# Performance work log

Hardware: AMD Instinct MI355X
Metric: run time of the kernel (lower is better)

The kernel has to match this reference:

```python
import jax, jax.numpy as jnp
import numpy as np
import math

S, B, D = 2048, 2, 1024
H = 16
DH = D // H
WIN = 256
DIL = 1


def setup_inputs() -> dict:
    key = jax.random.key(0)
    ks = jax.random.split(key, 10)
    std = 1.0 / math.sqrt(D)
    return {
        "x": jax.random.normal(ks[0], (S, B, D), jnp.float32),
        "beta": jax.random.normal(ks[1], (H,), jnp.float32) * 0.02,
        "Wq": jax.random.normal(ks[2], (D, D), jnp.float32) * std,
        "bq": jnp.zeros((D,), jnp.float32),
        "Wk": jax.random.normal(ks[3], (D, D), jnp.float32) * std,
        "bk": jnp.zeros((D,), jnp.float32),
        "Wv": jax.random.normal(ks[4], (D, D), jnp.float32) * std,
        "bv": jnp.zeros((D,), jnp.float32),
        "Wo": jax.random.normal(ks[5], (D, D), jnp.float32) * std,
        "bo": jnp.zeros((D,), jnp.float32),
    }


def _split_heads(t):
    # (S, B, D) -> (B*H, S, DH), matching rearrange 's b (h d) -> (b h) s d'
    return t.reshape(S, B, H, DH).transpose(1, 2, 0, 3).reshape(B * H, S, DH)


def reference(x, beta, Wq, bq, Wk, bk, Wv, bv, Wo, bo):
    q = _split_heads(x @ Wq + bq)
    k = _split_heads(x @ Wk + bk)
    v = _split_heads(x @ Wv + bv)

    # per-head learnable temperature: q / (sqrt(d_head) * exp(beta))
    beta_exp = jnp.tile(jnp.exp(beta), B)  # (B*H,), head index = z % H
    q = q / (jnp.sqrt(jnp.asarray(DH, x.dtype)) * beta_exp)[:, None, None]

    # causal dilated windowed mask
    idx = jnp.arange(S)
    diff = idx[:, None] - idx[None, :]
    allowed = (diff >= 0) & (diff <= DIL * (WIN - 1)) & (diff % DIL == 0)
    mask = jnp.where(allowed, jnp.asarray(0.0, x.dtype), jnp.asarray(-jnp.inf, x.dtype))

    scores = jnp.einsum('zqd,zkd->zqk', q, k) + mask[None]
    # attention sink: extra zero-logit column absorbing probability mass
    scores = jnp.concatenate([scores, jnp.zeros((B * H, S, 1), scores.dtype)], axis=-1)
    attn = jax.nn.softmax(scores, axis=-1)[..., :-1]

    out = jnp.einsum('zqk,zkd->zqd', attn, v)
    # (B*H, S, DH) -> (S, B, D)
    out = out.reshape(B, H, S, DH).transpose(2, 0, 1, 3).reshape(S, B, D)
    return out @ Wo + bo
```

## Files before the change

### kernel.cpp

```cpp
#include <hip/hip_runtime.h>
#include <math.h>

#define S_LEN  2048
#define BATCH  2
#define DM     1024
#define NHEAD  16
#define DHEAD  64
#define WIN    256
#define MROWS  4096

#define PPAD 68

#define BM 128
#define BN 96
#define BK 32
#define NKT (DM / BK)

#define OM 128
#define ON 64

typedef __attribute__((ext_vector_type(8))) short bf16x8;
typedef __attribute__((ext_vector_type(4))) float f32x4;

__device__ __forceinline__ unsigned short f2b(float f) {
    unsigned int u = __float_as_uint(f);
    return (unsigned short)((u + 0x7fffu + ((u >> 16) & 1u)) >> 16);
}
__device__ __forceinline__ void gld16(const void* g, void* l) {
    __builtin_amdgcn_global_load_lds(
        (const __attribute__((address_space(1))) void*)g,
        (__attribute__((address_space(3))) void*)l, 16, 0, 0);
}
__device__ __forceinline__ bf16x8 pack8(float4 a, float4 b) {
    bf16x8 r;
    r[0] = (short)f2b(a.x); r[1] = (short)f2b(a.y);
    r[2] = (short)f2b(a.z); r[3] = (short)f2b(a.w);
    r[4] = (short)f2b(b.x); r[5] = (short)f2b(b.y);
    r[6] = (short)f2b(b.z); r[7] = (short)f2b(b.w);
    return r;
}

__global__ __launch_bounds__(256)
void twcvt4(const float* __restrict__ W0, const float* __restrict__ W1,
            const float* __restrict__ W2, const float* __restrict__ W3,
            const float* __restrict__ x,
            unsigned short* __restrict__ T0, unsigned short* __restrict__ T1,
            unsigned short* __restrict__ T2, unsigned short* __restrict__ T3,
            unsigned short* __restrict__ xb)
{
    const int zz = blockIdx.z;
    if (zz == 4) {
        const int flat = blockIdx.y * 32 + blockIdx.x;
        const int base = flat * 4096 + threadIdx.x * 4;
#pragma unroll
        for (int p = 0; p < 4; ++p) {
            const int i = base + p * 1024;
            float4 f = *(const float4*)(x + i);
            ushort4 o;
            o.x = f2b(f.x); o.y = f2b(f.y); o.z = f2b(f.z); o.w = f2b(f.w);
            *(ushort4*)(xb + i) = o;
        }
        return;
    }
    const float* W = (zz == 0) ? W0 : (zz == 1) ? W1 : (zz == 2) ? W2 : W3;
    unsigned short* WT = (zz == 0) ? T0 : (zz == 1) ? T1 : (zz == 2) ? T2 : T3;

    __shared__ float t32[32][33];
    const int bx = blockIdx.x * 32;
    const int by = blockIdx.y * 32;
    const int c  = threadIdx.x & 31;
    const int r0 = threadIdx.x >> 5;
#pragma unroll
    for (int p = 0; p < 4; ++p)
        t32[r0 + 8 * p][c] = W[(size_t)(by + r0 + 8 * p) * DM + bx + c];
    __syncthreads();
#pragma unroll
    for (int p = 0; p < 4; ++p)
        WT[(size_t)(bx + r0 + 8 * p) * DM + by + c] = f2b(t32[c][r0 + 8 * p]);
}

__global__ __launch_bounds__(256, 4)
void gemm_qkv(const unsigned short* __restrict__ A,
              const unsigned short* __restrict__ BT,
              const float* __restrict__ b0,
              const float* __restrict__ b1,
              const float* __restrict__ b2,
              const float* __restrict__ beta,
              unsigned short* __restrict__ Cb)
{
    __shared__ unsigned short Ab[2][BM * BK];
    __shared__ unsigned short Bb[2][BN * BK];

    const int t   = threadIdx.x;
    const int ln  = t & 63;
    const int wv  = t >> 6;
    const int wr  = wv >> 1;
    const int wc  = wv & 1;
    const int m16 = ln & 15;
    const int g   = ln >> 4;
    const int swz = (m16 >> 1) & 3;

    const int rowBase = blockIdx.y * BM;
    const int colBase = blockIdx.x * BN;

    const int sr  = t >> 2;
    const int scx = (t & 3) ^ ((sr >> 1) & 3);
    const size_t gOff = (size_t)sr * DM + scx * 8;
    const int    ldOff = t * 8;

    f32x4 acc[4][3];
#pragma unroll
    for (int u = 0; u < 4; ++u)
#pragma unroll
        for (int v = 0; v < 3; ++v)
            acc[u][v] = (f32x4){0.f, 0.f, 0.f, 0.f};

    const unsigned short* aBase = A  + (size_t)rowBase * DM + gOff;
    const unsigned short* bBase = BT + (size_t)colBase * DM + gOff;

    {
        gld16(aBase,                    &Ab[0][ldOff]);
        gld16(aBase + (size_t)64 * DM,  &Ab[0][2048 + ldOff]);
        gld16(bBase,                    &Bb[0][ldOff]);
        if (t < 128)
            gld16(bBase + (size_t)64 * DM, &Bb[0][2048 + ldOff]);
        asm volatile("s_waitcnt vmcnt(0)" ::: "memory");
        __builtin_amdgcn_s_barrier();
        __builtin_amdgcn_sched_barrier(0);
    }

    for (int kt = 0; kt < NKT; ++kt) {
        const int cur = kt & 1;
        const unsigned short* Ac = Ab[cur];
        const unsigned short* Bc = Bb[cur];
        unsigned short* An = Ab[cur ^ 1];
        unsigned short* Bn = Bb[cur ^ 1];
        const bool hn = (kt < NKT - 1);
        const unsigned short* aS = aBase + (size_t)(kt + 1) * BK;
        const unsigned short* bS = bBase + (size_t)(kt + 1) * BK;

        if (hn) {
            gld16(aS,                   &An[ldOff]);
            gld16(aS + (size_t)64 * DM, &An[2048 + ldOff]);
            gld16(bS,                   &Bn[ldOff]);
            if (t < 128)
                gld16(bS + (size_t)64 * DM, &Bn[2048 + ldOff]);
        }

        bf16x8 af[4], bf[3];
#pragma unroll
        for (int u = 0; u < 4; ++u)
            af[u] = *(const bf16x8*)&Ac[(wr * 64 + u * 16 + m16) * BK + ((g ^ swz) * 8)];
#pragma unroll
        for (int v = 0; v < 3; ++v)
            bf[v] = *(const bf16x8*)&Bc[(wc * 48 + v * 16 + m16) * BK + ((g ^ swz) * 8)];

        __builtin_amdgcn_s_setprio(1);
#pragma unroll
        for (int u = 0; u < 4; ++u)
#pragma unroll
            for (int v = 0; v < 3; ++v)
                acc[u][v] = __builtin_amdgcn_mfma_f32_16x16x32_bf16(
                    af[u], bf[v], acc[u][v], 0, 0, 0);
        __builtin_amdgcn_s_setprio(0);

        if (hn)
            asm volatile("s_waitcnt vmcnt(0)" ::: "memory");
        __builtin_amdgcn_s_barrier();
        __builtin_amdgcn_sched_barrier(0);
    }

    const int q4 = g * 4;
#pragma unroll
    for (int v = 0; v < 3; ++v) {
        const int col = colBase + wc * 48 + v * 16 + m16;
        const int sec = col >> 10;
        const int h   = (col >> 6) & (NHEAD - 1);
        const int dh  = col & 63;
        if (sec < 2) {
            const float bi = (sec == 0 ? b0 : b1)[col & (DM - 1)];
            const float sc = (sec == 0) ? 0.125f * __expf(-beta[h]) : 1.0f;
            unsigned short* base = Cb + (size_t)sec * MROWS * DM;
#pragma unroll
            for (int u = 0; u < 4; ++u)
#pragma unroll
                for (int r = 0; r < 4; ++r) {
                    const int row = rowBase + wr * 64 + u * 16 + q4 + r;
                    const int s = row >> 1, bb = row & 1;
                    const int z = bb * NHEAD + h;
                    base[((size_t)z * S_LEN + s) * DHEAD + dh] =
                        f2b((acc[u][v][r] + bi) * sc);
                }
        } else {
            unsigned short* vtb = Cb + (size_t)2 * MROWS * DM;
            const float bi = b2[col & (DM - 1)];
#pragma unroll
            for (int u = 0; u < 4; ++u) {
                const int row0 = rowBase + wr * 64 + u * 16 + q4;
                const int s0   = row0 >> 1;
                ushort2 p0, p1;
                p0.x = f2b(acc[u][v][0] + bi);
                p0.y = f2b(acc[u][v][2] + bi);
                p1.x = f2b(acc[u][v][1] + bi);
                p1.y = f2b(acc[u][v][3] + bi);
                *(ushort2*)(vtb + ((size_t)(h * DHEAD + dh) * S_LEN + s0)) = p0;
                *(ushort2*)(vtb + ((size_t)((NHEAD + h) * DHEAD + dh) * S_LEN + s0)) = p1;
            }
        }
    }
}

__global__ __launch_bounds__(256, 2)
void gemm_out(const unsigned short* __restrict__ A,
              const unsigned short* __restrict__ BT,
              const float* __restrict__ bias,
              float* __restrict__ Cf)
{
    __shared__ unsigned short As[2][OM * 64];
    __shared__ unsigned short Bs[2][ON * 64];

    const int t  = threadIdx.x;
    const int wv = t >> 6, ln = t & 63;
    const int wr = wv >> 1, wc = wv & 1;
    const int m16 = ln & 15, g = ln >> 4;
    const int sw  = m16 & 7;

    const int rowBase = blockIdx.y * OM;
    const int colBase = blockIdx.x * ON;

    const int sr  = t >> 3;
    const int scx = (t & 7) ^ (sr & 7);
    const size_t gOff = (size_t)sr * DM + scx * 8;
    const int    ldOff = t * 8;

    f32x4 acc[4][2];
#pragma unroll
    for (int u = 0; u < 4; ++u)
#pragma unroll
        for (int v = 0; v < 2; ++v)
            acc[u][v] = (f32x4){0.f, 0.f, 0.f, 0.f};

    {
        const unsigned short* a0 = A  + (size_t)rowBase * DM + gOff;
        const unsigned short* bt = BT + (size_t)colBase * DM + gOff;
#pragma unroll
        for (int j = 0; j < 4; ++j)
            gld16(a0 + (size_t)(j * 32) * DM, &As[0][j * 2048 + ldOff]);
#pragma unroll
        for (int j = 0; j < 2; ++j)
            gld16(bt + (size_t)(j * 32) * DM, &Bs[0][j * 2048 + ldOff]);
        asm volatile("s_waitcnt vmcnt(0)" ::: "memory");
        __builtin_amdgcn_s_barrier();
        __builtin_amdgcn_sched_barrier(0);
    }

    for (int kt = 0; kt < DM / 64; ++kt) {
        const int cur = kt & 1;
        const unsigned short* Ac = As[cur];
        const unsigned short* Bc = Bs[cur];
        unsigned short* An = As[cur ^ 1];
        unsigned short* Bn = Bs[cur ^ 1];
        const bool hn = (kt < DM / 64 - 1);
        const unsigned short* aS = A  + (size_t)rowBase * DM + (kt + 1) * 64 + gOff;
        const unsigned short* bS = BT + (size_t)colBase * DM + (kt + 1) * 64 + gOff;

        bf16x8 af0[4], bf0[2];
#pragma unroll
        for (int u = 0; u < 4; ++u)
            af0[u] = *(const bf16x8*)&Ac[(wr * 64 + u * 16 + m16) * 64 + ((g ^ sw) * 8)];
#pragma unroll
        for (int v = 0; v < 2; ++v)
            bf0[v] = *(const bf16x8*)&Bc[(wc * 32 + v * 16 + m16) * 64 + ((g ^ sw) * 8)];

        if (hn) {
#pragma unroll
            for (int j = 0; j < 4; ++j)
                gld16(aS + (size_t)(j * 32) * DM, &An[j * 2048 + ldOff]);
#pragma unroll
            for (int j = 0; j < 2; ++j)
                gld16(bS + (size_t)(j * 32) * DM, &Bn[j * 2048 + ldOff]);
        }

        __builtin_amdgcn_s_setprio(1);
#pragma unroll
        for (int u = 0; u < 4; ++u)
#pragma unroll
            for (int v = 0; v < 2; ++v)
                acc[u][v] = __builtin_amdgcn_mfma_f32_16x16x32_bf16(
                    af0[u], bf0[v], acc[u][v], 0, 0, 0);
        __builtin_amdgcn_s_setprio(0);

        bf16x8 af1[4], bf1[2];
#pragma unroll
        for (int u = 0; u < 4; ++u)
            af1[u] = *(const bf16x8*)&Ac[(wr * 64 + u * 16 + m16) * 64 + (((4 | g) ^ sw) * 8)];
#pragma unroll
        for (int v = 0; v < 2; ++v)
            bf1[v] = *(const bf16x8*)&Bc[(wc * 32 + v * 16 + m16) * 64 + (((4 | g) ^ sw) * 8)];

        __builtin_amdgcn_s_setprio(1);
#pragma unroll
        for (int u = 0; u < 4; ++u)
#pragma unroll
            for (int v = 0; v < 2; ++v)
                acc[u][v] = __builtin_amdgcn_mfma_f32_16x16x32_bf16(
                    af1[u], bf1[v], acc[u][v], 0, 0, 0);
        __builtin_amdgcn_s_setprio(0);

        if (hn)
            asm volatile("s_waitcnt vmcnt(0)" ::: "memory");
        __builtin_amdgcn_s_barrier();
        __builtin_amdgcn_sched_barrier(0);
    }

    const int q4 = g * 4;
#pragma unroll
    for (int v = 0; v < 2; ++v) {
        const int col = colBase + wc * 32 + v * 16 + m16;
        const float bi = bias[col];
#pragma unroll
        for (int u = 0; u < 4; ++u)
#pragma unroll
            for (int r = 0; r < 4; ++r) {
                const int row = rowBase + wr * 64 + u * 16 + q4 + r;
                Cf[(size_t)row * DM + col] = acc[u][v][r] + bi;
            }
    }
}

__global__ __launch_bounds__(256, 3)
void attn_mfma(const unsigned short* __restrict__ q,
               const unsigned short* __restrict__ k,
               const unsigned short* __restrict__ vt,
               unsigned short* __restrict__ ao)
{
    __shared__ unsigned short Ks[2][64 * 64];
    __shared__ unsigned short Vs[2][64 * 64];
    __shared__ float Ps[64][PPAD];

    const int t   = threadIdx.x;
    const int wv  = t >> 6, ln = t & 63;
    const int m16 = ln & 15, g = ln >> 4;
    const int sw  = m16 & 7;
    const int z   = blockIdx.y;
    const int q0  = blockIdx.x * 64;
    const size_t zbase = (size_t)z * S_LEN * DHEAD;

    const int sr  = t >> 3;
    const int scx = (t & 7) ^ (sr & 7);
    const unsigned short* kS = k  + zbase + (size_t)sr * DHEAD + scx * 8;
    const unsigned short* vS = vt + ((size_t)z * DHEAD + sr) * S_LEN + scx * 8;
    const int ldOff = t * 8;

    const unsigned short* qrow = q + zbase + (size_t)(q0 + wv * 16 + m16) * DHEAD;
    bf16x8 qf0 = *(const bf16x8*)(qrow + g * 8);
    bf16x8 qf1 = *(const bf16x8*)(qrow + 32 + g * 8);

    f32x4 oacc[4];
#pragma unroll
    for (int v4 = 0; v4 < 4; ++v4) oacc[v4] = (f32x4){0.f, 0.f, 0.f, 0.f};
    float lr[4];
#pragma unroll
    for (int r = 0; r < 4; ++r) lr[r] = 1.f;

    const int c0 = (blockIdx.x < 4) ? (4 - (int)blockIdx.x) : 0;

    {
        const int kb = q0 - 256 + c0 * 64;
        gld16(kS + (size_t)kb * DHEAD,        &Ks[0][ldOff]);
        gld16(kS + (size_t)(kb + 32) * DHEAD, &Ks[0][2048 + ldOff]);
        gld16(vS + kb,                        &Vs[0][ldOff]);
        gld16(vS + (size_t)32 * S_LEN + kb,   &Vs[0][2048 + ldOff]);
        asm volatile("s_waitcnt vmcnt(0)" ::: "memory");
        __builtin_amdgcn_s_barrier();
        __builtin_amdgcn_sched_barrier(0);
    }

    for (int c = c0; c < 5; ++c) {
        const int cur = (c - c0) & 1;
        const int kb  = q0 - 256 + c * 64;
        const bool hn = (c < 4);

        if (hn) {
            const int kn = kb + 64;
            gld16(kS + (size_t)kn * DHEAD,        &Ks[cur ^ 1][ldOff]);
            gld16(kS + (size_t)(kn + 32) * DHEAD, &Ks[cur ^ 1][2048 + ldOff]);
            gld16(vS + kn,                        &Vs[cur ^ 1][ldOff]);
            gld16(vS + (size_t)32 * S_LEN + kn,   &Vs[cur ^ 1][2048 + ldOff]);
        }

        f32x4 sacc[4];
#pragma unroll
        for (int v4 = 0; v4 < 4; ++v4) {
            sacc[v4] = (f32x4){0.f, 0.f, 0.f, 0.f};
            bf16x8 kf0 = *(const bf16x8*)&Ks[cur][(v4 * 16 + m16) * 64 + ((g ^ sw) * 8)];
            sacc[v4] = __builtin_amdgcn_mfma_f32_16x16x32_bf16(qf0, kf0, sacc[v4], 0, 0, 0);
            bf16x8 kf1 = *(const bf16x8*)&Ks[cur][(v4 * 16 + m16) * 64 + (((4 | g) ^ sw) * 8)];
            sacc[v4] = __builtin_amdgcn_mfma_f32_16x16x32_bf16(qf1, kf1, sacc[v4], 0, 0, 0);
        }

        const bool mhi = (c == 4), mlo = (c == 0);
#pragma unroll
        for (int r = 0; r < 4; ++r) {
            const int ig = q0 + wv * 16 + g * 4 + r;
            float rsum = 0.f;
#pragma unroll
            for (int v4 = 0; v4 < 4; ++v4) {
                const int jg = kb + v4 * 16 + m16;
                float x = sacc[v4][r];
                const bool valid = (!mhi || jg <= ig) && (!mlo || jg >= ig - (WIN - 1));
                x = valid ? x : -1e30f;
                const float pp = __expf(x);
                Ps[wv * 16 + g * 4 + r][v4 * 16 + m16] = pp;
                rsum += pp;
            }
#pragma unroll
            for (int off = 1; off < 16; off <<= 1)
                rsum += __shfl_xor(rsum, off, 64);
            lr[r] += rsum;
        }

        asm volatile("s_waitcnt lgkmcnt(0)" ::: "memory");
        __builtin_amdgcn_sched_barrier(0);

        const float* prow = &Ps[wv * 16 + m16][0];
        bf16x8 pf0 = pack8(*(const float4*)(prow + g * 8),
                           *(const float4*)(prow + g * 8 + 4));
        bf16x8 pf1 = pack8(*(const float4*)(prow + 32 + g * 8),
                           *(const float4*)(prow + 32 + g * 8 + 4));
#pragma unroll
        for (int v4 = 0; v4 < 4; ++v4) {
            bf16x8 vf0 = *(const bf16x8*)&Vs[cur][(v4 * 16 + m16) * 64 + ((g ^ sw) * 8)];
            oacc[v4] = __builtin_amdgcn_mfma_f32_16x16x32_bf16(pf0, vf0, oacc[v4], 0, 0, 0);
            bf16x8 vf1 = *(const bf16x8*)&Vs[cur][(v4 * 16 + m16) * 64 + (((4 | g) ^ sw) * 8)];
            oacc[v4] = __builtin_amdgcn_mfma_f32_16x16x32_bf16(pf1, vf1, oacc[v4], 0, 0, 0);
        }

        if (hn) {
            asm volatile("s_waitcnt vmcnt(0)" ::: "memory");
            __builtin_amdgcn_s_barrier();
            __builtin_amdgcn_sched_barrier(0);
        }
    }

    const int bb = z >> 4, h = z & 15;
#pragma unroll
    for (int r = 0; r < 4; ++r) {
        const int ig  = q0 + wv * 16 + g * 4 + r;
        const float inv = 1.f / lr[r];
#pragma unroll
        for (int v4 = 0; v4 < 4; ++v4)
            ao[(size_t)(ig * BATCH + bb) * DM + h * DHEAD + v4 * 16 + m16] =
                f2b(oacc[v4][r] * inv);
    }
}

extern "C" void kernel_launch(void* const* d_in, const int* in_sizes, int n_in,
                              void* d_out, int out_size, void* d_ws, size_t ws_size,
                              hipStream_t stream)
{
    const float* x    = (const float*)d_in[0];
    const float* beta = (const float*)d_in[1];
    const float* Wq   = (const float*)d_in[2];
    const float* bq   = (const float*)d_in[3];
    const float* Wk   = (const float*)d_in[4];
    const float* bk   = (const float*)d_in[5];
    const float* Wv   = (const float*)d_in[6];
    const float* bv   = (const float*)d_in[7];
    const float* Wo   = (const float*)d_in[8];
    const float* bo   = (const float*)d_in[9];
    float* out = (float*)d_out;

    unsigned short* w = (unsigned short*)d_ws;
    const size_t seg = (size_t)MROWS * DM;
    unsigned short* qb  = w;
    unsigned short* kb  = w + seg;
    unsigned short* vtb = w + 2 * seg;
    unsigned short* ab  = w + 3 * seg;
    unsigned short* xb  = w + 4 * seg;
    unsigned short* wtq = w + 5 * seg;
    unsigned short* wtk = wtq + (size_t)DM * DM;
    unsigned short* wtv = wtk + (size_t)DM * DM;
    unsigned short* wto = wtv + (size_t)DM * DM;

    twcvt4<<<dim3(32, 32, 5), 256, 0, stream>>>(
        Wq, Wk, Wv, Wo, x, wtq, wtk, wtv, wto, xb);

    gemm_qkv<<<dim3(3072 / BN, MROWS / BM), 256, 0, stream>>>(
        xb, wtq, bq, bk, bv, beta, qb);

    attn_mfma<<<dim3(S_LEN / 64, BATCH * NHEAD), 256, 0, stream>>>(qb, kb, vtb, ab);

    gemm_out<<<dim3(DM / ON, MROWS / OM), 256, 0, stream>>>(ab, wto, bo, out);
}
```

Baseline: 175.7 us.

## Enlarge QKV GEMM tile to 256x256x64 with 8 waves and staged ping-pong loads

Raises the QKV projection GEMM tile from 128x96x32 to 256x256x64 and runs it with 512 threads (8 waves in a 2x4 layout). Each k-step is split into four MFMA quadrants, and the next tile's global-to-LDS loads are interleaved between them with partial vmcnt waits and barriers. The XOR swizzle is widened to 8 chunks. The aim is more data reuse per LDS byte and overlap of loads with MFMA work. The cost is a much smaller grid (12x16 = 192 blocks, under one wave on the CU count), higher register pressure from 128 accumulator floats per lane, and more barriers per k-step.

```diff
diff --git a/kernel.cpp b/kernel.cpp
--- a/kernel.cpp
+++ b/kernel.cpp
@@ -11,9 +11,9 @@
 
 #define PPAD 68
 
-#define BM 128
-#define BN 96
-#define BK 32
+#define BM 256
+#define BN 256
+#define BK 64
 #define NKT (DM / BK)
 
 #define OM 128
@@ -79,7 +79,7 @@
         WT[(size_t)(bx + r0 + 8 * p) * DM + by + c] = f2b(t32[c][r0 + 8 * p]);
 }
 
-__global__ __launch_bounds__(256, 4)
+__global__ __launch_bounds__(512, 2)
 void gemm_qkv(const unsigned short* __restrict__ A,
               const unsigned short* __restrict__ BT,
               const float* __restrict__ b0,
@@ -94,86 +94,160 @@
     const int t   = threadIdx.x;
     const int ln  = t & 63;
     const int wv  = t >> 6;
-    const int wr  = wv >> 1;
-    const int wc  = wv & 1;
+    const int wr  = wv >> 2;
+    const int wc  = wv & 3;
     const int m16 = ln & 15;
     const int g   = ln >> 4;
-    const int swz = (m16 >> 1) & 3;
+    const int sw  = m16 & 7;
 
     const int rowBase = blockIdx.y * BM;
     const int colBase = blockIdx.x * BN;
 
-    const int sr  = t >> 2;
-    const int scx = (t & 3) ^ ((sr >> 1) & 3);
+    const int sr  = t >> 3;
+    const int scx = (t & 7) ^ (sr & 7);
     const size_t gOff = (size_t)sr * DM + scx * 8;
     const int    ldOff = t * 8;
 
-    f32x4 acc[4][3];
-#pragma unroll
-    for (int u = 0; u < 4; ++u)
-#pragma unroll
-        for (int v = 0; v < 3; ++v)
-            acc[u][v] = (f32x4){0.f, 0.f, 0.f, 0.f};
-
     const unsigned short* aBase = A  + (size_t)rowBase * DM + gOff;
     const unsigned short* bBase = BT + (size_t)colBase * DM + gOff;
 
-    {
-        gld16(aBase,                    &Ab[0][ldOff]);
-        gld16(aBase + (size_t)64 * DM,  &Ab[0][2048 + ldOff]);
-        gld16(bBase,                    &Bb[0][ldOff]);
-        if (t < 128)
-            gld16(bBase + (size_t)64 * DM, &Bb[0][2048 + ldOff]);
-        asm volatile("s_waitcnt vmcnt(0)" ::: "memory");
-        __builtin_amdgcn_s_barrier();
-        __builtin_amdgcn_sched_barrier(0);
-    }
+    f32x4 acc[8][4];
+#pragma unroll
+    for (int u = 0; u < 8; ++u)
+#pragma unroll
+        for (int v = 0; v < 4; ++v)
+            acc[u][v] = (f32x4){0.f, 0.f, 0.f, 0.f};
+
+#define STAGE_AR(buf, kt1, r)                                                 \
+    gld16(aBase + (size_t)(kt1) * BK + (size_t)((r) * 64) * DM,               \
+          &Ab[buf][(r) * 4096 + ldOff])
+#define STAGE_BR(buf, kt1, r)                                                 \
+    gld16(bBase + (size_t)(kt1) * BK + (size_t)((r) * 64) * DM,               \
+          &Bb[buf][(r) * 4096 + ldOff])
+
+    STAGE_BR(0, 0, 0); STAGE_BR(0, 0, 1); STAGE_BR(0, 0, 2); STAGE_BR(0, 0, 3);
+    STAGE_AR(0, 0, 0); STAGE_AR(0, 0, 2);
+    STAGE_AR(0, 0, 1); STAGE_AR(0, 0, 3);
+    asm volatile("s_waitcnt vmcnt(2)" ::: "memory");
+    __builtin_amdgcn_s_barrier();
+    __builtin_amdgcn_sched_barrier(0);
+
+    bf16x8 afr[4][2], bfr[4][2];
 
     for (int kt = 0; kt < NKT; ++kt) {
-        const int cur = kt & 1;
+        const int cur = kt & 1, nxt = cur ^ 1;
         const unsigned short* Ac = Ab[cur];
         const unsigned short* Bc = Bb[cur];
-        unsigned short* An = Ab[cur ^ 1];
-        unsigned short* Bn = Bb[cur ^ 1];
         const bool hn = (kt < NKT - 1);
-        const unsigned short* aS = aBase + (size_t)(kt + 1) * BK;
-        const unsigned short* bS = bBase + (size_t)(kt + 1) * BK;
-
-        if (hn) {
-            gld16(aS,                   &An[ldOff]);
-            gld16(aS + (size_t)64 * DM, &An[2048 + ldOff]);
-            gld16(bS,                   &Bn[ldOff]);
-            if (t < 128)
-                gld16(bS + (size_t)64 * DM, &Bn[2048 + ldOff]);
-        }
-
-        bf16x8 af[4], bf[3];
-#pragma unroll
-        for (int u = 0; u < 4; ++u)
-            af[u] = *(const bf16x8*)&Ac[(wr * 64 + u * 16 + m16) * BK + ((g ^ swz) * 8)];
-#pragma unroll
-        for (int v = 0; v < 3; ++v)
-            bf[v] = *(const bf16x8*)&Bc[(wc * 48 + v * 16 + m16) * BK + ((g ^ swz) * 8)];
-
+
+#pragma unroll
+        for (int u = 0; u < 4; ++u) {
+            const int ro = (wr * 128 + u * 16 + m16) * BK;
+            afr[u][0] = *(const bf16x8*)&Ac[ro + ((g ^ sw) * 8)];
+            afr[u][1] = *(const bf16x8*)&Ac[ro + (((4 | g) ^ sw) * 8)];
+        }
+#pragma unroll
+        for (int v = 0; v < 2; ++v) {
+            const int ro = (wc * 64 + v * 16 + m16) * BK;
+            bfr[v][0] = *(const bf16x8*)&Bc[ro + ((g ^ sw) * 8)];
+            bfr[v][1] = *(const bf16x8*)&Bc[ro + (((4 | g) ^ sw) * 8)];
+        }
+        if (hn) { STAGE_BR(nxt, kt + 1, 0); STAGE_BR(nxt, kt + 1, 1); }
+        __builtin_amdgcn_s_barrier();
+        asm volatile("s_waitcnt lgkmcnt(0)" ::: "memory");
+        __builtin_amdgcn_sched_barrier(0);
         __builtin_amdgcn_s_setprio(1);
 #pragma unroll
         for (int u = 0; u < 4; ++u)
 #pragma unroll
-            for (int v = 0; v < 3; ++v)
+            for (int v = 0; v < 2; ++v) {
                 acc[u][v] = __builtin_amdgcn_mfma_f32_16x16x32_bf16(
-                    af[u], bf[v], acc[u][v], 0, 0, 0);
+                    afr[u][0], bfr[v][0], acc[u][v], 0, 0, 0);
+                acc[u][v] = __builtin_amdgcn_mfma_f32_16x16x32_bf16(
+                    afr[u][1], bfr[v][1], acc[u][v], 0, 0, 0);
+            }
         __builtin_amdgcn_s_setprio(0);
-
+        __builtin_amdgcn_s_barrier();
+        __builtin_amdgcn_sched_barrier(0);
+
+#pragma unroll
+        for (int v = 0; v < 2; ++v) {
+            const int ro = (wc * 64 + 32 + v * 16 + m16) * BK;
+            bfr[2 + v][0] = *(const bf16x8*)&Bc[ro + ((g ^ sw) * 8)];
+            bfr[2 + v][1] = *(const bf16x8*)&Bc[ro + (((4 | g) ^ sw) * 8)];
+        }
+        if (hn) { STAGE_BR(nxt, kt + 1, 2); STAGE_BR(nxt, kt + 1, 3); }
+        __builtin_amdgcn_s_barrier();
+        asm volatile("s_waitcnt lgkmcnt(0)" ::: "memory");
+        __builtin_amdgcn_sched_barrier(0);
+        __builtin_amdgcn_s_setprio(1);
+#pragma unroll
+        for (int u = 0; u < 4; ++u)
+#pragma unroll
+            for (int v = 0; v < 2; ++v) {
+                acc[u][2 + v] = __builtin_amdgcn_mfma_f32_16x16x32_bf16(
+                    afr[u][0], bfr[2 + v][0], acc[u][2 + v], 0, 0, 0);
+                acc[u][2 + v] = __builtin_amdgcn_mfma_f32_16x16x32_bf16(
+                    afr[u][1], bfr[2 + v][1], acc[u][2 + v], 0, 0, 0);
+            }
+        __builtin_amdgcn_s_setprio(0);
         if (hn)
+            asm volatile("s_waitcnt vmcnt(4)" ::: "memory");
+        else
             asm volatile("s_waitcnt vmcnt(0)" ::: "memory");
         __builtin_amdgcn_s_barrier();
         __builtin_amdgcn_sched_barrier(0);
-    }
+
+#pragma unroll
+        for (int u = 0; u < 4; ++u) {
+            const int ro = (wr * 128 + 64 + u * 16 + m16) * BK;
+            afr[u][0] = *(const bf16x8*)&Ac[ro + ((g ^ sw) * 8)];
+            afr[u][1] = *(const bf16x8*)&Ac[ro + (((4 | g) ^ sw) * 8)];
+        }
+        if (hn) { STAGE_AR(nxt, kt + 1, 0); STAGE_AR(nxt, kt + 1, 2); }
+        __builtin_amdgcn_s_barrier();
+        asm volatile("s_waitcnt lgkmcnt(0)" ::: "memory");
+        __builtin_amdgcn_sched_barrier(0);
+        __builtin_amdgcn_s_setprio(1);
+#pragma unroll
+        for (int u = 0; u < 4; ++u)
+#pragma unroll
+            for (int v = 0; v < 2; ++v) {
+                acc[4 + u][2 + v] = __builtin_amdgcn_mfma_f32_16x16x32_bf16(
+                    afr[u][0], bfr[2 + v][0], acc[4 + u][2 + v], 0, 0, 0);
+                acc[4 + u][2 + v] = __builtin_amdgcn_mfma_f32_16x16x32_bf16(
+                    afr[u][1], bfr[2 + v][1], acc[4 + u][2 + v], 0, 0, 0);
+            }
+        __builtin_amdgcn_s_setprio(0);
+        __builtin_amdgcn_s_barrier();
+        __builtin_amdgcn_sched_barrier(0);
+
+        if (hn) { STAGE_AR(nxt, kt + 1, 1); STAGE_AR(nxt, kt + 1, 3); }
+        __builtin_amdgcn_s_barrier();
+        __builtin_amdgcn_sched_barrier(0);
+        __builtin_amdgcn_s_setprio(1);
+#pragma unroll
+        for (int u = 0; u < 4; ++u)
+#pragma unroll
+            for (int v = 0; v < 2; ++v) {
+                acc[4 + u][v] = __builtin_amdgcn_mfma_f32_16x16x32_bf16(
+                    afr[u][0], bfr[v][0], acc[4 + u][v], 0, 0, 0);
+                acc[4 + u][v] = __builtin_amdgcn_mfma_f32_16x16x32_bf16(
+                    afr[u][1], bfr[v][1], acc[4 + u][v], 0, 0, 0);
+            }
+        __builtin_amdgcn_s_setprio(0);
+        if (hn)
+            asm volatile("s_waitcnt vmcnt(2)" ::: "memory");
+        __builtin_amdgcn_s_barrier();
+        __builtin_amdgcn_sched_barrier(0);
+    }
+#undef STAGE_AR
+#undef STAGE_BR
 
     const int q4 = g * 4;
 #pragma unroll
-    for (int v = 0; v < 3; ++v) {
-        const int col = colBase + wc * 48 + v * 16 + m16;
+    for (int v = 0; v < 4; ++v) {
+        const int col = colBase + wc * 64 + v * 16 + m16;
         const int sec = col >> 10;
         const int h   = (col >> 6) & (NHEAD - 1);
         const int dh  = col & 63;
@@ -182,10 +256,10 @@
             const float sc = (sec == 0) ? 0.125f * __expf(-beta[h]) : 1.0f;
             unsigned short* base = Cb + (size_t)sec * MROWS * DM;
 #pragma unroll
-            for (int u = 0; u < 4; ++u)
+            for (int u = 0; u < 8; ++u)
 #pragma unroll
                 for (int r = 0; r < 4; ++r) {
-                    const int row = rowBase + wr * 64 + u * 16 + q4 + r;
+                    const int row = rowBase + wr * 128 + u * 16 + q4 + r;
                     const int s = row >> 1, bb = row & 1;
                     const int z = bb * NHEAD + h;
                     base[((size_t)z * S_LEN + s) * DHEAD + dh] =
@@ -195,8 +269,8 @@
             unsigned short* vtb = Cb + (size_t)2 * MROWS * DM;
             const float bi = b2[col & (DM - 1)];
 #pragma unroll
-            for (int u = 0; u < 4; ++u) {
-                const int row0 = rowBase + wr * 64 + u * 16 + q4;
+            for (int u = 0; u < 8; ++u) {
+                const int row0 = rowBase + wr * 128 + u * 16 + q4;
                 const int s0   = row0 >> 1;
                 ushort2 p0, p1;
                 p0.x = f2b(acc[u][v][0] + bi);
@@ -486,7 +560,7 @@
     twcvt4<<<dim3(32, 32, 5), 256, 0, stream>>>(
         Wq, Wk, Wv, Wo, x, wtq, wtk, wtv, wto, xb);
 
-    gemm_qkv<<<dim3(3072 / BN, MROWS / BM), 256, 0, stream>>>(
+    gemm_qkv<<<dim3(3072 / BN, MROWS / BM), 512, 0, stream>>>(
         xb, wtq, bq, bk, bv, beta, qb);
 
     attn_mfma<<<dim3(S_LEN / 64, BATCH * NHEAD), 256, 0, stream>>>(qb, kb, vtb, ab);
```

Result: no change. 174.8 us (-0.5%).
